# Performance work log

Hardware: AMD Instinct MI355X
Metric: run time of the kernel (lower is better)

Reference implementation:

```python
import jax, jax.numpy as jnp
import numpy as np

B, S, D, H = 1, 2048, 4096, 32
HD = D // H  # 128


def _rope_params(seq_len, head_dim, base=10000.0):
    inv_freq = 1.0 / (base ** (np.arange(0, head_dim, 2, dtype=np.float64) / head_dim))
    ang = np.outer(np.arange(seq_len, dtype=np.float64), inv_freq)      # [S, HD/2]
    ang = np.concatenate([ang, ang], axis=-1)                            # [S, HD]
    return jnp.asarray(np.cos(ang), jnp.float32), jnp.asarray(np.sin(ang), jnp.float32)


def _apply_rope(x, cos, sin):
    # x: [B, H, S, HD]; cos/sin: [S, HD]
    half = x.shape[-1] // 2
    x1, x2 = x[..., :half], x[..., half:]
    rotated = jnp.concatenate([-x2, x1], axis=-1)
    return x * cos[None, None] + rotated * sin[None, None]


def setup_inputs() -> dict:
    key = jax.random.key(0)
    ks = jax.random.split(key, 6)
    w_scale = 1.0 / np.sqrt(D)
    X = jax.random.normal(ks[0], (B, S, D), jnp.float32)
    Wq = jax.random.normal(ks[1], (D, D), jnp.float32) * w_scale
    Wk = jax.random.normal(ks[2], (D, D), jnp.float32) * w_scale
    Wv = jax.random.normal(ks[3], (D, D), jnp.float32) * w_scale
    Wo = jax.random.normal(ks[4], (D, D), jnp.float32) * w_scale
    bo = jax.random.normal(ks[5], (D,), jnp.float32) * 0.01
    cos, sin = _rope_params(S, HD)
    return {"X": X, "Wq": Wq, "Wk": Wk, "Wv": Wv, "Wo": Wo, "bo": bo, "cos": cos, "sin": sin}


def reference(X, Wq, Wk, Wv, Wo, bo, cos, sin):
    b, s, d = X.shape
    # nn.Linear: y = x @ W.T
    def split_heads(y):
        return y.reshape(b, s, H, HD).transpose(0, 2, 1, 3)  # [B,H,S,HD]
    q = split_heads(X @ Wq.T)
    k = split_heads(X @ Wk.T)
    v = split_heads(X @ Wv.T)
    q = _apply_rope(q, cos, sin)
    k = _apply_rope(k, cos, sin)
    scores = jnp.einsum('bhqd,bhkd->bhqk', q, k) / np.sqrt(HD).astype(np.float32)
    causal = jnp.tril(jnp.ones((s, s), bool))
    scores = jnp.where(causal[None, None], scores, -jnp.inf)
    attn = jax.nn.softmax(scores, axis=-1)
    out = jnp.einsum('bhqk,bhkd->bhqd', attn, v)  # [B,H,S,HD]
    out = out.transpose(0, 2, 1, 3).reshape(b, s, d)
    return out @ Wo.T + bo
```

## Files before the change

kernel.cpp:

```cpp
#include <hip/hip_runtime.h>

typedef unsigned short u16;
typedef __attribute__((ext_vector_type(8))) short s16x8;
typedef __attribute__((ext_vector_type(4))) float f32x4;

__device__ __forceinline__ u16 f2bf(float f) {
  unsigned u = __float_as_uint(f);
  u += 0x7fffu + ((u >> 16) & 1u);
  return (u16)(u >> 16);
}
__device__ __forceinline__ float bf2f(u16 h) {
  return __uint_as_float(((unsigned)h) << 16);
}

typedef __attribute__((address_space(1))) const void gvoid_t;
typedef __attribute__((address_space(3))) void lvoid_t;
__device__ __forceinline__ void gload_lds16(const void* g, void* l) {
  __builtin_amdgcn_global_load_lds((gvoid_t*)g, (lvoid_t*)l, 16, 0, 0);
}

__global__ void cvt_f32_bf16(const float* __restrict__ in, u16* __restrict__ out, int n) {
  int i = (blockIdx.x * 256 + threadIdx.x) * 4;
  if (i >= n) return;
  float4 v = *(const float4*)(in + i);
  ushort4 o;
  o.x = f2bf(v.x); o.y = f2bf(v.y); o.z = f2bf(v.z); o.w = f2bf(v.w);
  *(ushort4*)(out + i) = o;
}

template<typename OutT, bool BIAS>
__global__ __launch_bounds__(256) void gemm_bt3(
    const u16* __restrict__ A, const u16* __restrict__ Bm,
    OutT* __restrict__ C, const float* __restrict__ bias,
    int M, int N, int K)
{
  __shared__ u16 As[3][128 * 32];
  __shared__ u16 Bs[3][128 * 32];

  const int t = threadIdx.x;
  const int lane = t & 63, wid = t >> 6;
  const int wm = wid >> 1, wn = wid & 1;
  const int lr = lane & 15, lk = lane >> 4;

  const int wg = blockIdx.x;
  const int xcd = wg & 7, j = wg >> 3;
  const int m0 = (j & 15) * 128;
  const int n0 = ((xcd << 2) | (j >> 4)) * 128;

  const int nt = K >> 5;

  f32x4 acc[4][4] = {};

#define STAGE3(KT)                                                             \
  {                                                                            \
    const int bu_ = (KT) % 3;                                                  \
    const int k0_ = (KT) << 5;                                                 \
    _Pragma("unroll")                                                          \
    for (int it = 0; it < 2; ++it) {                                           \
      int id = it * 256 + t;                                                   \
      int r = id >> 2, c0 = id & 3;                                            \
      int cs = (c0 ^ ((r >> 1) & 3)) << 3;                                     \
      gload_lds16(A + (size_t)(m0 + r) * K + k0_ + cs, &As[bu_][id * 8]);      \
      gload_lds16(Bm + (size_t)(n0 + r) * K + k0_ + cs, &Bs[bu_][id * 8]);     \
    }                                                                          \
  }

  STAGE3(0);
  STAGE3(1);
  asm volatile("s_waitcnt vmcnt(4)" ::: "memory");
  __builtin_amdgcn_s_barrier();

  for (int kt = 0; kt < nt; ++kt) {
    const int bu = kt % 3;
    if (kt + 2 < nt) STAGE3(kt + 2);

    s16x8 af[4], bf[4];
#pragma unroll
    for (int i = 0; i < 4; ++i) {
      int ra = wm * 64 + i * 16 + lr;
      af[i] = *(const s16x8*)&As[bu][ra * 32 + ((lk ^ ((ra >> 1) & 3)) << 3)];
      int rb = wn * 64 + i * 16 + lr;
      bf[i] = *(const s16x8*)&Bs[bu][rb * 32 + ((lk ^ ((rb >> 1) & 3)) << 3)];
    }
    __builtin_amdgcn_s_setprio(1);
#pragma unroll
    for (int i = 0; i < 4; ++i)
#pragma unroll
      for (int jn = 0; jn < 4; ++jn)
        acc[i][jn] = __builtin_amdgcn_mfma_f32_16x16x32_bf16(af[i], bf[jn], acc[i][jn], 0, 0, 0);
    __builtin_amdgcn_s_setprio(0);

    asm volatile("s_waitcnt lgkmcnt(0)" ::: "memory");
    if (kt + 2 < nt)       { asm volatile("s_waitcnt vmcnt(4)" ::: "memory"); }
    else if (kt + 2 == nt) { asm volatile("s_waitcnt vmcnt(0)" ::: "memory"); }
    if (kt + 1 < nt) __builtin_amdgcn_s_barrier();
  }
#undef STAGE3

#pragma unroll
  for (int i = 0; i < 4; ++i) {
    int row_b = m0 + wm * 64 + i * 16 + lk * 4;
#pragma unroll
    for (int jn = 0; jn < 4; ++jn) {
      int col = n0 + wn * 64 + jn * 16 + lr;
      float bv = BIAS ? bias[col] : 0.f;
#pragma unroll
      for (int r = 0; r < 4; ++r) {
        float v = acc[i][jn][r] + bv;
        size_t off = (size_t)(row_b + r) * N + col;
        if constexpr (sizeof(OutT) == 2) ((u16*)C)[off] = f2bf(v);
        else                             ((float*)C)[off] = v;
      }
    }
  }
}

__global__ void rope_qk(u16* __restrict__ Q, u16* __restrict__ Kt,
                        const float* __restrict__ cosp, const float* __restrict__ sinp) {
  int i = blockIdx.x * 256 + threadIdx.x;
  int d = i & 63;
  int h = (i >> 6) & 31;
  int s = i >> 11;
  float c = cosp[s * 128 + d], sn = sinp[s * 128 + d];
  size_t base = (size_t)s * 4096 + h * 128 + d;
  float q1 = bf2f(Q[base]), q2 = bf2f(Q[base + 64]);
  Q[base]      = f2bf(q1 * c - q2 * sn);
  Q[base + 64] = f2bf(q2 * c + q1 * sn);
  float k1 = bf2f(Kt[base]), k2 = bf2f(Kt[base + 64]);
  Kt[base]      = f2bf(k1 * c - k2 * sn);
  Kt[base + 64] = f2bf(k2 * c + k1 * sn);
}

__global__ __launch_bounds__(512) void flash_attn(
    const u16* __restrict__ Q, const u16* __restrict__ Kg, const u16* __restrict__ Vg,
    u16* __restrict__ Ctx)
{
  const int D = 4096;
  __shared__ u16 Ks[2][64 * 128];
  __shared__ u16 Vt[128 * 64];
  __shared__ u16 Ps[8][16 * 64];

  const int t = threadIdx.x, lane = t & 63, wid = t >> 6;
  const int lr = lane & 15, lk = lane >> 4;

  const int wg = blockIdx.x;
  const int xcd = wg & 7, j = wg >> 3;
  const int bx = 15 - (j >> 2);
  const int h = xcd * 4 + (j & 3);
  const int q0 = bx * 128;
  const int qw0 = q0 + wid * 16;

  s16x8 qf[4];
#pragma unroll
  for (int kc = 0; kc < 4; ++kc)
    qf[kc] = *(const s16x8*)(Q + (size_t)(qw0 + lr) * D + h * 128 + kc * 32 + lk * 8);

  f32x4 o[8] = {};
  float m_r[4] = {-1e30f, -1e30f, -1e30f, -1e30f};
  float l_r[4] = {0.f, 0.f, 0.f, 0.f};

  const int ntiles = 2 * bx + 2;
  const float scale2 = 0.12751779f;

  const int ch = t & 15, kv2 = (t >> 4) * 2;

  {
    const u16* src = Vg + (size_t)kv2 * D + h * 128 + ch * 8;
    s16x8 a0 = *(const s16x8*)src;
    s16x8 a1 = *(const s16x8*)(src + D);
#pragma unroll
    for (int it = 0; it < 2; ++it) {
      int id = it * 512 + t;
      int kv = id >> 4, c0 = id & 15;
      gload_lds16(Kg + (size_t)kv * D + h * 128 + ((c0 ^ (kv & 7)) << 3), &Ks[0][id * 8]);
    }
#pragma unroll
    for (int jj = 0; jj < 8; ++jj) {
      int d = ch * 8 + jj;
      int sw = ((ch ^ jj) & 7) << 3;
      unsigned pr = (unsigned)(u16)a0[jj] | ((unsigned)(u16)a1[jj] << 16);
      *(unsigned*)&Vt[d * 64 + (kv2 ^ sw)] = pr;
    }
  }

  for (int kt = 0; kt < ntiles; ++kt) {
    const int b = kt & 1;
    const int kv0 = kt * 64;
    __syncthreads();

    s16x8 a0, a1;
    const bool pf = (kt + 1 < ntiles);
    if (pf) {
      const u16* src = Vg + (size_t)(kv0 + 64 + kv2) * D + h * 128 + ch * 8;
      a0 = *(const s16x8*)src;
      a1 = *(const s16x8*)(src + D);
#pragma unroll
      for (int it = 0; it < 2; ++it) {
        int id = it * 512 + t;
        int kv = id >> 4, c0 = id & 15;
        gload_lds16(Kg + (size_t)(kv0 + 64 + kv) * D + h * 128 + ((c0 ^ (kv & 7)) << 3),
                    &Ks[b ^ 1][id * 8]);
      }
    }

    if (kv0 <= qw0 + 15) {
      const bool masked = (kv0 + 63 > qw0);

      f32x4 st[4] = {};
      __builtin_amdgcn_s_setprio(1);
#pragma unroll
      for (int nt = 0; nt < 4; ++nt) {
        int kv = nt * 16 + lr;
        int sw = kv & 7;
#pragma unroll
        for (int kc = 0; kc < 4; ++kc) {
          s16x8 kf = *(const s16x8*)&Ks[b][kv * 128 + (((4 * kc + lk) ^ sw) << 3)];
          st[nt] = __builtin_amdgcn_mfma_f32_16x16x32_bf16(qf[kc], kf, st[nt], 0, 0, 0);
        }
      }
      __builtin_amdgcn_s_setprio(0);

      float pmax_[4];
#pragma unroll
      for (int r = 0; r < 4; ++r) {
        int q_r = qw0 + lk * 4 + r;
        if (masked) {
#pragma unroll
          for (int nt = 0; nt < 4; ++nt) {
            float sv = st[nt][r] * scale2;
            if (kv0 + nt * 16 + lr > q_r) sv = -1e30f;
            st[nt][r] = sv;
          }
        } else {
#pragma unroll
          for (int nt = 0; nt < 4; ++nt) st[nt][r] *= scale2;
        }
        float pm = fmaxf(fmaxf(st[0][r], st[1][r]), fmaxf(st[2][r], st[3][r]));
        pm = fmaxf(pm, __shfl_xor(pm, 1));
        pm = fmaxf(pm, __shfl_xor(pm, 2));
        pm = fmaxf(pm, __shfl_xor(pm, 4));
        pm = fmaxf(pm, __shfl_xor(pm, 8));
        pmax_[r] = pm;
      }
      bool nr = (pmax_[0] > m_r[0] + 8.f) || (pmax_[1] > m_r[1] + 8.f) ||
                (pmax_[2] > m_r[2] + 8.f) || (pmax_[3] > m_r[3] + 8.f);
      if (__any(nr)) {
#pragma unroll
        for (int r = 0; r < 4; ++r) {
          float mn = fmaxf(m_r[r], pmax_[r]);
          float al = __builtin_amdgcn_exp2f(m_r[r] - mn);
          m_r[r] = mn; l_r[r] *= al;
#pragma unroll
          for (int nb = 0; nb < 8; ++nb) o[nb][r] *= al;
        }
      }
#pragma unroll
      for (int r = 0; r < 4; ++r) {
        int ql = lk * 4 + r;
        int swp = ((ql >> 1) & 7) << 3;
        float ps = 0.f;
#pragma unroll
        for (int nt = 0; nt < 4; ++nt) {
          float pv = __builtin_amdgcn_exp2f(st[nt][r] - m_r[r]);
          ps += pv;
          Ps[wid][ql * 64 + ((nt * 16 + lr) ^ swp)] = f2bf(pv);
        }
        ps += __shfl_xor(ps, 1);
        ps += __shfl_xor(ps, 2);
        ps += __shfl_xor(ps, 4);
        ps += __shfl_xor(ps, 8);
        l_r[r] += ps;
      }
      asm volatile("s_waitcnt lgkmcnt(0)" ::: "memory");

      s16x8 pa[2];
#pragma unroll
      for (int ks = 0; ks < 2; ++ks) {
        int col = (ks * 32 + lk * 8) ^ (((lr >> 1) & 7) << 3);
        pa[ks] = *(const s16x8*)&Ps[wid][lr * 64 + col];
      }

      __builtin_amdgcn_s_setprio(1);
#pragma unroll
      for (int ks = 0; ks < 2; ++ks) {
#pragma unroll
        for (int nb = 0; nb < 8; ++nb) {
          int d = nb * 16 + lr;
          int g = (((d >> 3) ^ d) & 7) << 3;
          s16x8 vf = *(const s16x8*)&Vt[d * 64 + ((ks * 32 + lk * 8) ^ g)];
          o[nb] = __builtin_amdgcn_mfma_f32_16x16x32_bf16(pa[ks], vf, o[nb], 0, 0, 0);
        }
      }
      __builtin_amdgcn_s_setprio(0);
    }

    if (pf) {
      __builtin_amdgcn_s_barrier();
#pragma unroll
      for (int jj = 0; jj < 8; ++jj) {
        int d = ch * 8 + jj;
        int sw = ((ch ^ jj) & 7) << 3;
        unsigned pr = (unsigned)(u16)a0[jj] | ((unsigned)(u16)a1[jj] << 16);
        *(unsigned*)&Vt[d * 64 + (kv2 ^ sw)] = pr;
      }
    }
  }

#pragma unroll
  for (int r = 0; r < 4; ++r) {
    float inv = 1.f / l_r[r];
    int q_r = qw0 + lk * 4 + r;
#pragma unroll
    for (int nb = 0; nb < 8; ++nb)
      Ctx[(size_t)q_r * D + h * 128 + nb * 16 + lr] = f2bf(o[nb][r] * inv);
  }
}

extern "C" void kernel_launch(void* const* d_in, const int* in_sizes, int n_in,
                              void* d_out, int out_size, void* d_ws, size_t ws_size,
                              hipStream_t stream) {
  const int S = 2048, D = 4096, H = 32;
  const size_t SD = (size_t)S * D, DD = (size_t)D * D;

  const float* X  = (const float*)d_in[0];
  const float* Wq = (const float*)d_in[1];
  const float* Wk = (const float*)d_in[2];
  const float* Wv = (const float*)d_in[3];
  const float* Wo = (const float*)d_in[4];
  const float* bo = (const float*)d_in[5];
  const float* cs = (const float*)d_in[6];
  const float* sn = (const float*)d_in[7];

  u16* WB = (u16*)d_ws;
  u16* Xb = WB + DD;
  u16* Qb = Xb + SD;
  u16* Kb = Qb + SD;
  u16* Vb = Kb + SD;

  dim3 blk(256);
  dim3 g3(512);
  dim3 b3(256);

  cvt_f32_bf16<<<(int)(SD / 1024), blk, 0, stream>>>(X, Xb, (int)SD);
  cvt_f32_bf16<<<(int)(DD / 1024), blk, 0, stream>>>(Wq, WB, (int)DD);
  gemm_bt3<u16, false><<<g3, b3, 0, stream>>>(Xb, WB, Qb, nullptr, S, D, D);
  cvt_f32_bf16<<<(int)(DD / 1024), blk, 0, stream>>>(Wk, WB, (int)DD);
  gemm_bt3<u16, false><<<g3, b3, 0, stream>>>(Xb, WB, Kb, nullptr, S, D, D);
  cvt_f32_bf16<<<(int)(DD / 1024), blk, 0, stream>>>(Wv, WB, (int)DD);
  gemm_bt3<u16, false><<<g3, b3, 0, stream>>>(Xb, WB, Vb, nullptr, S, D, D);

  rope_qk<<<(S * H * 64) / 256, blk, 0, stream>>>(Qb, Kb, cs, sn);

  flash_attn<<<dim3(512), dim3(512), 0, stream>>>(Qb, Kb, Vb, Xb );

  cvt_f32_bf16<<<(int)(DD / 1024), blk, 0, stream>>>(Wo, WB, (int)DD);
  gemm_bt3<float, true><<<g3, b3, 0, stream>>>(Xb, WB, (float*)d_out, bo, S, D, D);
}
```

Baseline: 574.2 us.

## Fuse Q/K/V projections into one stacked-weight GEMM launch

```diff
diff --git a/kernel.cpp b/kernel.cpp
--- a/kernel.cpp
+++ b/kernel.cpp
@@ -111,6 +111,92 @@
         if constexpr (sizeof(OutT) == 2) ((u16*)C)[off] = f2bf(v);
         else                             ((float*)C)[off] = v;
       }
+    }
+  }
+}
+
+__global__ __launch_bounds__(256) void gemm_qkv(
+    const u16* __restrict__ A, const u16* __restrict__ Bstk,
+    u16* __restrict__ Qb, u16* __restrict__ Kb, u16* __restrict__ Vb,
+    int M, int K)
+{
+  __shared__ u16 As[3][128 * 32];
+  __shared__ u16 Bs[3][128 * 32];
+
+  const int t = threadIdx.x;
+  const int lane = t & 63, wid = t >> 6;
+  const int wm = wid >> 1, wn = wid & 1;
+  const int lr = lane & 15, lk = lane >> 4;
+
+  const int wg = blockIdx.x;
+  const int xcd = wg & 7, j = wg >> 3;
+  const int m0 = (j & 15) * 128;
+  const int n0 = (xcd * 12 + (j >> 4)) * 128;
+
+  const int nt = K >> 5;
+
+  f32x4 acc[4][4] = {};
+
+#define STAGEQ(KT)                                                             \
+  {                                                                            \
+    const int bu_ = (KT) % 3;                                                  \
+    const int k0_ = (KT) << 5;                                                 \
+    _Pragma("unroll")                                                          \
+    for (int it = 0; it < 2; ++it) {                                           \
+      int id = it * 256 + t;                                                   \
+      int r = id >> 2, c0 = id & 3;                                            \
+      int cs = (c0 ^ ((r >> 1) & 3)) << 3;                                     \
+      gload_lds16(A + (size_t)(m0 + r) * K + k0_ + cs, &As[bu_][id * 8]);      \
+      gload_lds16(Bstk + (size_t)(n0 + r) * K + k0_ + cs, &Bs[bu_][id * 8]);   \
+    }                                                                          \
+  }
+
+  STAGEQ(0);
+  STAGEQ(1);
+  asm volatile("s_waitcnt vmcnt(4)" ::: "memory");
+  __builtin_amdgcn_s_barrier();
+
+  for (int kt = 0; kt < nt; ++kt) {
+    const int bu = kt % 3;
+    if (kt + 2 < nt) STAGEQ(kt + 2);
+
+    s16x8 af[4], bf[4];
+#pragma unroll
+    for (int i = 0; i < 4; ++i) {
+      int ra = wm * 64 + i * 16 + lr;
+      af[i] = *(const s16x8*)&As[bu][ra * 32 + ((lk ^ ((ra >> 1) & 3)) << 3)];
+      int rb = wn * 64 + i * 16 + lr;
+      bf[i] = *(const s16x8*)&Bs[bu][rb * 32 + ((lk ^ ((rb >> 1) & 3)) << 3)];
+    }
+    __builtin_amdgcn_s_setprio(1);
+#pragma unroll
+    for (int i = 0; i < 4; ++i)
+#pragma unroll
+      for (int jn = 0; jn < 4; ++jn)
+        acc[i][jn] = __builtin_amdgcn_mfma_f32_16x16x32_bf16(af[i], bf[jn], acc[i][jn], 0, 0, 0);
+    __builtin_amdgcn_s_setprio(0);
+
+    asm volatile("s_waitcnt lgkmcnt(0)" ::: "memory");
+    if (kt + 2 < nt)       { asm volatile("s_waitcnt vmcnt(4)" ::: "memory"); }
+    else if (kt + 2 == nt) { asm volatile("s_waitcnt vmcnt(0)" ::: "memory"); }
+    if (kt + 1 < nt) __builtin_amdgcn_s_barrier();
+  }
+#undef STAGEQ
+
+  u16* Cp; int nb;
+  if (n0 < 4096)      { Cp = Qb; nb = n0; }
+  else if (n0 < 8192) { Cp = Kb; nb = n0 - 4096; }
+  else                { Cp = Vb; nb = n0 - 8192; }
+
+#pragma unroll
+  for (int i = 0; i < 4; ++i) {
+    int row_b = m0 + wm * 64 + i * 16 + lk * 4;
+#pragma unroll
+    for (int jn = 0; jn < 4; ++jn) {
+      int col = nb + wn * 64 + jn * 16 + lr;
+#pragma unroll
+      for (int r = 0; r < 4; ++r)
+        Cp[(size_t)(row_b + r) * 4096 + col] = f2bf(acc[i][jn][r]);
     }
   }
 }
@@ -145,7 +231,7 @@
 
   const int wg = blockIdx.x;
   const int xcd = wg & 7, j = wg >> 3;
-  const int bx = 15 - (j >> 2);
+  const int bx = (j < 32) ? (15 - (j >> 2)) : ((j - 32) >> 2);
   const int h = xcd * 4 + (j & 3);
   const int q0 = bx * 128;
   const int qw0 = q0 + wid * 16;
@@ -331,28 +417,50 @@
   const float* cs = (const float*)d_in[6];
   const float* sn = (const float*)d_in[7];
 
-  u16* WB = (u16*)d_ws;
-  u16* Xb = WB + DD;
-  u16* Qb = Xb + SD;
-  u16* Kb = Qb + SD;
-  u16* Vb = Kb + SD;
-
   dim3 blk(256);
   dim3 g3(512);
   dim3 b3(256);
 
-  cvt_f32_bf16<<<(int)(SD / 1024), blk, 0, stream>>>(X, Xb, (int)SD);
-  cvt_f32_bf16<<<(int)(DD / 1024), blk, 0, stream>>>(Wq, WB, (int)DD);
-  gemm_bt3<u16, false><<<g3, b3, 0, stream>>>(Xb, WB, Qb, nullptr, S, D, D);
-  cvt_f32_bf16<<<(int)(DD / 1024), blk, 0, stream>>>(Wk, WB, (int)DD);
-  gemm_bt3<u16, false><<<g3, b3, 0, stream>>>(Xb, WB, Kb, nullptr, S, D, D);
-  cvt_f32_bf16<<<(int)(DD / 1024), blk, 0, stream>>>(Wv, WB, (int)DD);
-  gemm_bt3<u16, false><<<g3, b3, 0, stream>>>(Xb, WB, Vb, nullptr, S, D, D);
-
-  rope_qk<<<(S * H * 64) / 256, blk, 0, stream>>>(Qb, Kb, cs, sn);
-
-  flash_attn<<<dim3(512), dim3(512), 0, stream>>>(Qb, Kb, Vb, Xb );
-
-  cvt_f32_bf16<<<(int)(DD / 1024), blk, 0, stream>>>(Wo, WB, (int)DD);
-  gemm_bt3<float, true><<<g3, b3, 0, stream>>>(Xb, WB, (float*)d_out, bo, S, D, D);
-}
+  const size_t need_fused = (3 * DD + 4 * SD) * sizeof(u16);
+
+  if (ws_size >= need_fused) {
+    u16* WB3 = (u16*)d_ws;
+    u16* Xb  = WB3 + 3 * DD;
+    u16* Qb  = Xb + SD;
+    u16* Kb  = Qb + SD;
+    u16* Vb  = Kb + SD;
+
+    cvt_f32_bf16<<<(int)(SD / 1024), blk, 0, stream>>>(X, Xb, (int)SD);
+    cvt_f32_bf16<<<(int)(DD / 1024), blk, 0, stream>>>(Wq, WB3, (int)DD);
+    cvt_f32_bf16<<<(int)(DD / 1024), blk, 0, stream>>>(Wk, WB3 + DD, (int)DD);
+    cvt_f32_bf16<<<(int)(DD / 1024), blk, 0, stream>>>(Wv, WB3 + 2 * DD, (int)DD);
+
+    gemm_qkv<<<dim3(1536), b3, 0, stream>>>(Xb, WB3, Qb, Kb, Vb, S, D);
+
+    rope_qk<<<(S * H * 64) / 256, blk, 0, stream>>>(Qb, Kb, cs, sn);
+    flash_attn<<<dim3(512), dim3(512), 0, stream>>>(Qb, Kb, Vb, Xb );
+
+    cvt_f32_bf16<<<(int)(DD / 1024), blk, 0, stream>>>(Wo, WB3, (int)DD);
+    gemm_bt3<float, true><<<g3, b3, 0, stream>>>(Xb, WB3, (float*)d_out, bo, S, D, D);
+  } else {
+    u16* WB = (u16*)d_ws;
+    u16* Xb = WB + DD;
+    u16* Qb = Xb + SD;
+    u16* Kb = Qb + SD;
+    u16* Vb = Kb + SD;
+
+    cvt_f32_bf16<<<(int)(SD / 1024), blk, 0, stream>>>(X, Xb, (int)SD);
+    cvt_f32_bf16<<<(int)(DD / 1024), blk, 0, stream>>>(Wq, WB, (int)DD);
+    gemm_bt3<u16, false><<<g3, b3, 0, stream>>>(Xb, WB, Qb, nullptr, S, D, D);
+    cvt_f32_bf16<<<(int)(DD / 1024), blk, 0, stream>>>(Wk, WB, (int)DD);
+    gemm_bt3<u16, false><<<g3, b3, 0, stream>>>(Xb, WB, Kb, nullptr, S, D, D);
+    cvt_f32_bf16<<<(int)(DD / 1024), blk, 0, stream>>>(Wv, WB, (int)DD);
+    gemm_bt3<u16, false><<<g3, b3, 0, stream>>>(Xb, WB, Vb, nullptr, S, D, D);
+
+    rope_qk<<<(S * H * 64) / 256, blk, 0, stream>>>(Qb, Kb, cs, sn);
+    flash_attn<<<dim3(512), dim3(512), 0, stream>>>(Qb, Kb, Vb, Xb );
+
+    cvt_f32_bf16<<<(int)(DD / 1024), blk, 0, stream>>>(Wo, WB, (int)DD);
+    gemm_bt3<float, true><<<g3, b3, 0, stream>>>(Xb, WB, (float*)d_out, bo, S, D, D);
+  }
+}
```

Result: faster. 529.0 us (-7.9%).
